# Performance work log

Hardware: AMD Instinct MI355X
Metric: run time of the kernel (lower is better)

The kernel has to match this reference:

```python
import jax, jax.numpy as jnp
import numpy as np
from jax import lax

PART = 224   # PART_IMAGE_SIZE
PAD = 224    # PAD_SIZE
TOPN = 4
IOU_THRESH = 0.25
N_ANCHORS = 1614


def _conv(x, w, b, stride, pad):
    y = lax.conv_general_dilated(x, w, (stride, stride), [(pad, pad), (pad, pad)],
                                 dimension_numbers=('NCHW', 'OIHW', 'NCHW'))
    return y + b[None, :, None, None]


def _iou(box, boxes):
    # box [4], boxes [N,4] as (y0,x0,y1,x1)
    yy0 = jnp.maximum(box[0], boxes[:, 0]); xx0 = jnp.maximum(box[1], boxes[:, 1])
    yy1 = jnp.minimum(box[2], boxes[:, 2]); xx1 = jnp.minimum(box[3], boxes[:, 3])
    inter = jnp.clip(yy1 - yy0, 0.0) * jnp.clip(xx1 - xx0, 0.0)
    a = (box[2] - box[0]) * (box[3] - box[1])
    areas = (boxes[:, 2] - boxes[:, 0]) * (boxes[:, 3] - boxes[:, 1])
    return inter / (a + areas - inter)


def _nms(scores, boxes):
    # hard NMS keeping TOPN boxes; returns indices [TOPN]
    valid = jnp.ones(scores.shape, dtype=bool)
    idxs = []
    for _ in range(TOPN):
        i = jnp.argmax(jnp.where(valid, scores, -jnp.inf))
        idxs.append(i)
        valid = valid & (_iou(boxes[i], boxes) <= IOU_THRESH)
    return jnp.stack(idxs)


def _crop_resize(img, box):
    # img [3,Hp,Wp] padded image, box [4] float; bilinear, align_corners=True,
    # matching F.interpolate(x_pad[:, :, y0:y1, x0:x1], (PART, PART))
    Hp, Wp = img.shape[1], img.shape[2]
    def coords(c0, c1, L):
        t = jnp.arange(PART, dtype=img.dtype) / (PART - 1)
        c = c0 + (c1 - 1.0 - c0) * t          # absolute source coordinate
        cf = jnp.floor(c)
        lo = jnp.clip(cf.astype(jnp.int32), 0, L - 1)
        hi = jnp.clip(lo + 1, 0, L - 1)
        return lo, hi, c - cf
    yl, yh, wy = coords(box[0], box[2], Hp)
    xl, xh, wx = coords(box[1], box[3], Wp)
    g = lambda yi, xi: img[:, yi[:, None], xi[None, :]]   # [3,PART,PART]
    return ((1 - wy)[:, None] * ((1 - wx) * g(yl, xl) + wx * g(yl, xh))
            + wy[:, None] * ((1 - wx) * g(yh, xl) + wx * g(yh, xh)))


def setup_inputs() -> dict:
    key = jax.random.key(0)
    ks = jax.random.split(key, 20)
    x = jax.random.uniform(ks[0], (16, 3, 448, 448), dtype=jnp.float32)
    rpn_feature = jax.random.normal(ks[1], (16, 2048, 14, 14), dtype=jnp.float32)
    # valid boxes inside the padded 896x896 image
    y0 = jax.random.randint(ks[2], (N_ANCHORS,), 0, 560)
    x0 = jax.random.randint(ks[3], (N_ANCHORS,), 0, 560)
    h = jax.random.randint(ks[4], (N_ANCHORS,), 32, 336)
    w = jax.random.randint(ks[5], (N_ANCHORS,), 32, 336)
    anchors = jnp.stack([y0, x0, jnp.minimum(y0 + h, 896), jnp.minimum(x0 + w, 896)], axis=1).astype(jnp.int32)
    s = 0.02
    inp = {
        'x': x, 'rpn_feature': rpn_feature, 'anchors': anchors,
        'w_down1': jax.random.normal(ks[6], (128, 2048, 3, 3), jnp.float32) * s,
        'b_down1': jnp.zeros((128,), jnp.float32),
        'w_down2': jax.random.normal(ks[7], (128, 128, 3, 3), jnp.float32) * s,
        'b_down2': jnp.zeros((128,), jnp.float32),
        'w_down3': jax.random.normal(ks[8], (128, 128, 3, 3), jnp.float32) * s,
        'b_down3': jnp.zeros((128,), jnp.float32),
        'w_tidy1': jax.random.normal(ks[9], (6, 128, 1, 1), jnp.float32) * s,
        'b_tidy1': jnp.zeros((6,), jnp.float32),
        'w_tidy2': jax.random.normal(ks[10], (6, 128, 1, 1), jnp.float32) * s,
        'b_tidy2': jnp.zeros((6,), jnp.float32),
        'w_tidy3': jax.random.normal(ks[11], (9, 128, 1, 1), jnp.float32) * s,
        'b_tidy3': jnp.zeros((9,), jnp.float32),
    }
    return inp


def reference(x, rpn_feature, anchors,
              w_down1, b_down1, w_down2, b_down2, w_down3, b_down3,
              w_tidy1, b_tidy1, w_tidy2, b_tidy2, w_tidy3, b_tidy3):
    B = x.shape[0]
    # ProposalNet
    d1 = jax.nn.relu(_conv(rpn_feature, w_down1, b_down1, 1, 1))   # [B,128,14,14]
    d2 = jax.nn.relu(_conv(d1, w_down2, b_down2, 2, 1))            # [B,128,7,7]
    d3 = jax.nn.relu(_conv(d2, w_down3, b_down3, 2, 1))            # [B,128,4,4]
    t1 = _conv(d1, w_tidy1, b_tidy1, 1, 0).reshape(B, -1)
    t2 = _conv(d2, w_tidy2, b_tidy2, 1, 0).reshape(B, -1)
    t3 = _conv(d3, w_tidy3, b_tidy3, 1, 0).reshape(B, -1)
    rpn_score = jnp.concatenate([t1, t2, t3], axis=1)              # [B, 1614]
    boxes = anchors.astype(x.dtype)                                # [N,4]
    top_n_index = jax.vmap(lambda s: _nms(s, boxes))(rpn_score)    # [B,TOPN]
    top_n_prob = jnp.take_along_axis(rpn_score, top_n_index, axis=1)
    x_pad = jnp.pad(x, ((0, 0), (0, 0), (PAD, PAD), (PAD, PAD)))   # [B,3,896,896]
    sel_boxes = boxes[top_n_index]                                 # [B,TOPN,4]
    part_imgs = jax.vmap(lambda img, bxs: jax.vmap(lambda b: _crop_resize(img, b))(bxs))(x_pad, sel_boxes)
    # part_imgs: [B,TOPN,3,PART,PART]
    return rpn_score, top_n_index, top_n_prob, part_imgs
```

## Files before the change

### kernel.cpp

```cpp
#include <hip/hip_runtime.h>
#include <hip/hip_bf16.h>

#define NB 16
#define NA 1614
#define NBP (NB * 196 * 128)

typedef __bf16 bf16x8 __attribute__((ext_vector_type(8)));
typedef float f32x4 __attribute__((ext_vector_type(4)));

__device__ __forceinline__ unsigned short f2bf(float v) {
  unsigned u = __float_as_uint(v);
  unsigned r = (u + 0x7FFFu + ((u >> 16) & 1u)) >> 16;
  return (unsigned short)r;
}
__device__ __forceinline__ float bf2f(unsigned short s) {
  return __uint_as_float(((unsigned)s) << 16);
}

__global__ __launch_bounds__(256)
void prep(const float* __restrict__ w, const float* __restrict__ in,
          unsigned short* __restrict__ wTh, unsigned short* __restrict__ wTl,
          unsigned short* __restrict__ aTh, unsigned short* __restrict__ aTl) {
  __shared__ float sbuf[32 * 289];
  const int bid = blockIdx.x;
  if (bid < 1024) {
    const int chunk = bid & 63, b = bid >> 6;
    const float* src = in + ((size_t)b * 2048 + chunk * 32) * 196;
#pragma unroll
    for (int r = 0; r < 7; r++) {
      int e = threadIdx.x + 256 * r;
      if (e < 1568) {
        int ic = e / 49, f = e - ic * 49;
        float4 v = ((const float4*)(src + (size_t)ic * 196))[f];
        float* d = sbuf + ic * 201 + f * 4;
        d[0] = v.x; d[1] = v.y; d[2] = v.z; d[3] = v.w;
      }
    }
    __syncthreads();
    unsigned short* oh = aTh + (size_t)bid * (196 * 32);
    unsigned short* ol = aTl + (size_t)bid * (196 * 32);
#pragma unroll
    for (int r = 0; r < 4; r++) {
      int e = threadIdx.x + 256 * r;
      if (e < 784) {
        int pos = e >> 2, part = e & 3;
        unsigned short hv[8], lv[8];
#pragma unroll
        for (int j = 0; j < 8; j++) {
          float v = sbuf[(part * 8 + j) * 201 + pos];
          unsigned short h = f2bf(v);
          hv[j] = h;
          lv[j] = f2bf(v - bf2f(h));
        }
        ((uint4*)oh)[e] = *(uint4*)hv;
        ((uint4*)ol)[e] = *(uint4*)lv;
      }
    }
  } else {
    const int bid2 = bid - 1024;
    const int ocg = bid2 & 3, ks = (bid2 >> 2) & 3, kcp = bid2 >> 4;
    const int oc0 = ocg * 32;
    const int ic0 = kcp * 128 + ks * 32;
#pragma unroll
    for (int r = 0; r < 9; r++) {
      int f = threadIdx.x + 256 * r;
      int o = f / 72, rem4 = f - o * 72;
      float4 v = *(const float4*)(w + ((size_t)(oc0 + o) * 2048 + ic0) * 9 + rem4 * 4);
      float* d = sbuf + o * 289 + rem4 * 4;
      d[0] = v.x; d[1] = v.y; d[2] = v.z; d[3] = v.w;
    }
    __syncthreads();
#pragma unroll
    for (int r = 0; r < 36; r++) {
      int e = threadIdx.x + 256 * r;
      int tap = e >> 10, rem = e & 1023;
      int o = rem >> 5, ic = rem & 31;
      float v = sbuf[o * 289 + ic * 9 + tap];
      unsigned short h = f2bf(v);
      size_t g2 = ((size_t)(kcp * 36 + tap * 4 + ks) << 12) + oc0 * 32 + rem;
      wTh[g2] = h;
      wTl[g2] = f2bf(v - bf2f(h));
    }
  }
}

#define LOADB(H, L, T, K)                                                     \
  {                                                                           \
    const size_t o_ = ((size_t)(kc * 36 + (T) * 4 + (K)) << 12) + bln;        \
    const unsigned short* ph_ = wTh + o_;                                     \
    const unsigned short* pq_ = wTl + o_;                                     \
    H[0] = *(const bf16x8*)(ph_);                                             \
    H[1] = *(const bf16x8*)(ph_ + 512);                                       \
    H[2] = *(const bf16x8*)(ph_ + 1024);                                      \
    H[3] = *(const bf16x8*)(ph_ + 1536);                                      \
    L[0] = *(const bf16x8*)(pq_);                                             \
    L[1] = *(const bf16x8*)(pq_ + 512);                                       \
    L[2] = *(const bf16x8*)(pq_ + 1024);                                      \
    L[3] = *(const bf16x8*)(pq_ + 1536);                                      \
  }

#define STEP(IT, BUH, BUL, BNH, BNL)                                          \
  {                                                                           \
    const int it_ = (IT);                                                     \
    const int ks_ = it_ / 9, tap_ = it_ - ks_ * 9;                            \
    const int dy_ = tap_ / 3 - 1;                                             \
    const int dx_ = tap_ - (tap_ / 3) * 3 - 1;                                \
    const int td_ = (ks_ * 196 + dy_ * 14 + dx_) * 4;        \
    bf16x8 afh[7], afl[7];                                                    \
    _Pragma("unroll") for (int mf = 0; mf < 7; mf++) {                        \
      uint4 vh_ = gA0h[td_ + aoff[mf]];                                       \
      uint4 vl_ = gA0l[td_ + aoff[mf]];                                       \
      bool ok_ = ((unsigned)(ay[mf] + dy_) < 14u) &&                          \
                 ((unsigned)(ax[mf] + dx_) < 14u);                            \
      if (!ok_) {                                                             \
        vh_.x = 0u; vh_.y = 0u; vh_.z = 0u; vh_.w = 0u;                       \
        vl_.x = 0u; vl_.y = 0u; vl_.z = 0u; vl_.w = 0u;                       \
      }                                                                       \
      afh[mf] = *(const bf16x8*)&vh_;                                         \
      afl[mf] = *(const bf16x8*)&vl_;                                         \
    }                                                                         \
    {             \
      const int ni_ = (it_ < 35) ? it_ + 1 : 35;                              \
      const int nk_ = ni_ / 9, nt_ = ni_ - nk_ * 9;                           \
      LOADB(BNH, BNL, nt_, nk_);                                              \
    }                                                                         \
    _Pragma("unroll") for (int mf = 0; mf < 7; mf++)                          \
      _Pragma("unroll") for (int nf = 0; nf < 4; nf++)                        \
        acc[mf][nf] = __builtin_amdgcn_mfma_f32_16x16x32_bf16(afh[mf], BUH[nf], acc[mf][nf], 0, 0, 0); \
    _Pragma("unroll") for (int mf = 0; mf < 7; mf++)                          \
      _Pragma("unroll") for (int nf = 0; nf < 4; nf++)                        \
        acc[mf][nf] = __builtin_amdgcn_mfma_f32_16x16x32_bf16(afl[mf], BUH[nf], acc[mf][nf], 0, 0, 0); \
    _Pragma("unroll") for (int mf = 0; mf < 7; mf++)                          \
      _Pragma("unroll") for (int nf = 0; nf < 4; nf++)                        \
        acc[mf][nf] = __builtin_amdgcn_mfma_f32_16x16x32_bf16(afh[mf], BUL[nf], acc[mf][nf], 0, 0, 0); \
  }

__global__ __launch_bounds__(256, 1)
void conv1_mfma(const unsigned short* __restrict__ aTh, const unsigned short* __restrict__ aTl,
                const unsigned short* __restrict__ wTh, const unsigned short* __restrict__ wTl,
                float* __restrict__ p1) {
  const int bid = blockIdx.x;
  const int kc = bid & 15;
  const int b  = bid >> 4;
  const int tid = threadIdx.x;
  const int wid = tid >> 6, lane = tid & 63;
  const int wm = wid & 1, wn = wid >> 1;
  const int q = lane >> 4, ln = lane & 15;

  int ay[7], ax[7], aoff[7];
#pragma unroll
  for (int mf = 0; mf < 7; mf++) {
    int row = wm * 112 + mf * 16 + ln;
    int v = (row < 196);
    int y = v ? row / 14 : 0;
    int x = v ? (row - y * 14) : 0;
    if (!v) y = 0;
    ay[mf] = y; ax[mf] = x;
    aoff[mf] = (y * 14 + x) * 4 + q;
  }
  const int bln = (wn * 64 + ln) * 32 + q * 8;

  const uint4* gA0h = (const uint4*)(aTh + (size_t)(b * 64 + kc * 4) * 6272);
  const uint4* gA0l = (const uint4*)(aTl + (size_t)(b * 64 + kc * 4) * 6272);

  f32x4 acc[7][4];
#pragma unroll
  for (int mf = 0; mf < 7; mf++)
#pragma unroll
    for (int nf = 0; nf < 4; nf++) acc[mf][nf] = (f32x4){0.f, 0.f, 0.f, 0.f};

  bf16x8 b0h[4], b0l[4], b1h[4], b1l[4];
  LOADB(b0h, b0l, 0, 0);

  for (int it = 0; it < 36; it += 2) {
    STEP(it,     b0h, b0l, b1h, b1l);
    STEP(it + 1, b1h, b1l, b0h, b0l);
  }

  float* pk = p1 + ((size_t)kc * NB + b) * 196 * 128;
#pragma unroll
  for (int mf = 0; mf < 7; mf++) {
    const int row0 = wm * 112 + mf * 16 + q * 4;
#pragma unroll
    for (int nf = 0; nf < 4; nf++) {
      const int oc = wn * 64 + nf * 16 + ln;
#pragma unroll
      for (int r = 0; r < 4; r++) {
        const int row = row0 + r;
        if (row < 196) pk[(size_t)row * 128 + oc] = acc[mf][nf][r];
      }
    }
  }
}

__global__ __launch_bounds__(256)
void conv1_finish_p(const float* __restrict__ p1, const float* __restrict__ bias,
                    float* __restrict__ d1) {
  __shared__ float s[28 * 132];
  const int bid = blockIdx.x;
  const int pt = bid % 7, b = bid / 7;
  const int tid = threadIdx.x;
#pragma unroll
  for (int r = 0; r < 4; r++) {
    int u = tid + 256 * r;
    if (u < 896) {
      int pos = u >> 5, oc4 = u & 31;
      const float* base = p1 + ((size_t)(b * 196 + pt * 28 + pos)) * 128 + oc4 * 4;
      float4 sum = ((const float4*)bias)[oc4];
#pragma unroll
      for (int k = 0; k < 16; k++) {
        float4 v = *(const float4*)(base + (size_t)k * NBP);
        sum.x += v.x; sum.y += v.y; sum.z += v.z; sum.w += v.w;
      }
      sum.x = fmaxf(sum.x, 0.f); sum.y = fmaxf(sum.y, 0.f);
      sum.z = fmaxf(sum.z, 0.f); sum.w = fmaxf(sum.w, 0.f);
      *(float4*)(s + pos * 132 + oc4 * 4) = sum;
    }
  }
  __syncthreads();
#pragma unroll
  for (int r = 0; r < 4; r++) {
    int u = tid + 256 * r;
    if (u < 896) {
      int oc = u / 7, f = u - oc * 7;
      float4 v;
      v.x = s[(f * 4 + 0) * 132 + oc];
      v.y = s[(f * 4 + 1) * 132 + oc];
      v.z = s[(f * 4 + 2) * 132 + oc];
      v.w = s[(f * 4 + 3) * 132 + oc];
      *(float4*)(d1 + ((size_t)b * 128 + oc) * 196 + pt * 28 + f * 4) = v;
    }
  }
}

__global__ void conv2_part(const float* __restrict__ d1, const float* __restrict__ w,
                           float* __restrict__ p2) {
  const int bid = blockIdx.x;
  const int kc = bid & 3, oct = (bid >> 2) & 3, b = bid >> 4;
  const int ic0 = kc * 32, oc0 = oct * 32;
  const int tid = threadIdx.x;
  const int ocl = tid >> 3, rw = tid & 7;

  __shared__ float s_in[32 * 320];
  __shared__ float s_w[32 * 324];

#pragma unroll
  for (int r = 0; r < 32; r++) {
    const int e = tid + 256 * r;
    const int ch = e >> 8, idx = e & 255;
    const int tr = idx >> 4, tc = idx & 15;
    const int iy = tr - 1, ix = tc - 1;
    float v = 0.f;
    if ((unsigned)iy < 14u && (unsigned)ix < 14u)
      v = d1[((size_t)b * 128 + ic0 + ch) * 196 + iy * 14 + ix];
    s_in[ch * 320 + tr * 20 + tc] = v;
  }
#pragma unroll
  for (int r = 0; r < 36; r++) {
    const int e = tid + 256 * r;
    const int oc = e / 288, rem = e - oc * 288;
    const int ch = rem / 9, tap = rem - ch * 9;
    s_w[ch * 324 + tap * 36 + oc] =
        w[(size_t)(oc0 + oc) * 1152 + (size_t)ic0 * 9 + rem];
  }
  __syncthreads();

  if (rw < 7) {
    float acc[7] = {};
    for (int ic = 0; ic < 32; ic++) {
      const float* wrow = s_w + ic * 324 + ocl;
      const float* irow = s_in + ic * 320;
#pragma unroll
      for (int ky = 0; ky < 3; ky++) {
        const float* r = irow + (2 * rw + ky) * 20;
        const float4 f0 = *(const float4*)(r);
        const float4 f1 = *(const float4*)(r + 4);
        const float4 f2 = *(const float4*)(r + 8);
        const float4 f3 = *(const float4*)(r + 12);
        const float ev[8] = {f0.x, f0.z, f1.x, f1.z, f2.x, f2.z, f3.x, f3.z};
        const float od[7] = {f0.y, f0.w, f1.y, f1.w, f2.y, f2.w, f3.y};
        const float w0 = wrow[(ky * 3 + 0) * 36];
        const float w1 = wrow[(ky * 3 + 1) * 36];
        const float w2 = wrow[(ky * 3 + 2) * 36];
#pragma unroll
        for (int x = 0; x < 7; x++)
          acc[x] = fmaf(w0, ev[x], fmaf(w1, od[x], fmaf(w2, ev[x + 1], acc[x])));
      }
    }
    float* po = p2 + (((size_t)kc * NB + b) * 128 + oc0 + ocl) * 49 + rw * 7;
#pragma unroll
    for (int x = 0; x < 7; x++) po[x] = acc[x];
  }
}

__global__ void conv2_finish(const float* __restrict__ p2, const float* __restrict__ bias,
                             float* __restrict__ d2) {
  const int i = blockIdx.x * 256 + threadIdx.x;
  if (i >= NB * 128 * 49) return;
  const int oc = (i / 49) & 127;
  float s = bias[oc];
#pragma unroll
  for (int k = 0; k < 4; k++) s += p2[(size_t)k * (NB * 128 * 49) + i];
  d2[i] = fmaxf(s, 0.f);
}

__global__ void conv3_part(const float* __restrict__ d2, const float* __restrict__ w,
                           float* __restrict__ p3) {
  const int bid = blockIdx.x;
  const int kc = bid & 1, oct = (bid >> 1) & 7, b = bid >> 4;
  const int ic0 = kc * 64, oc0 = oct * 16;
  const int tid = threadIdx.x;
  const int oc = tid >> 4, p = tid & 15;
  const int y = p >> 2, x = p & 3;

  __shared__ float s_in[64 * 108];
  __shared__ float s_w[64 * 144];

#pragma unroll
  for (int r = 0; r < 21; r++) {
    const int e = tid + 256 * r;
    if (e < 64 * 81) {
      const int ch = e / 81, idx = e - ch * 81;
      const int tr = idx / 9, tc = idx - tr * 9;
      const int iy = tr - 1, ix = tc - 1;
      float v = 0.f;
      if ((unsigned)iy < 7u && (unsigned)ix < 7u)
        v = d2[((size_t)b * 128 + ic0 + ch) * 49 + iy * 7 + ix];
      s_in[ch * 108 + tr * 12 + tc] = v;
    }
  }
#pragma unroll
  for (int r = 0; r < 36; r++) {
    const int e = tid + 256 * r;
    const int o = e / 576, rem = e - o * 576;
    const int ch = rem / 9, tap = rem - ch * 9;
    s_w[ch * 144 + tap * 16 + o] =
        w[(size_t)(oc0 + o) * 1152 + (size_t)ic0 * 9 + rem];
  }
  __syncthreads();

  float acc = 0.f;
  for (int ic = 0; ic < 64; ic++) {
    const float* wrow = s_w + ic * 144 + oc;
    const float* irow = s_in + ic * 108 + 2 * y * 12 + 2 * x;
#pragma unroll
    for (int ky = 0; ky < 3; ky++)
#pragma unroll
      for (int kx = 0; kx < 3; kx++)
        acc = fmaf(wrow[(ky * 3 + kx) * 16], irow[ky * 12 + kx], acc);
  }
  p3[(((size_t)kc * NB + b) * 128 + oc0 + oc) * 16 + p] = acc;
}

__global__ __launch_bounds__(256, 1)
void score_nms(const float* __restrict__ d1, const float* __restrict__ d2,
               const float* __restrict__ p3, const float* __restrict__ bd3,
               const float* __restrict__ w1, const float* __restrict__ b1,
               const float* __restrict__ w2, const float* __restrict__ b2,
               const float* __restrict__ w3, const float* __restrict__ b3,
               const int* __restrict__ anchors, float* __restrict__ score,
               float* __restrict__ out_idx, float* __restrict__ out_prob,
               float* __restrict__ sel) {
  __shared__ float s_in[32 * 200];
  __shared__ float s_w[21 * 128];
  __shared__ float s_b[21];
  __shared__ float s_sc[NA];
  __shared__ float s_bx[NA * 4];
  __shared__ float r_s[256];
  __shared__ int r_i[256];
  const int b = blockIdx.x, tid = threadIdx.x;

  for (int i = tid; i < 768; i += 256) s_w[i] = w1[i];
  for (int i = tid; i < 768; i += 256) s_w[768 + i] = w2[i];
  for (int i = tid; i < 1152; i += 256) s_w[1536 + i] = w3[i];
  if (tid < 21) s_b[tid] = (tid < 6) ? b1[tid] : (tid < 12) ? b2[tid - 6] : b3[tid - 12];
  for (int i = tid; i < NA; i += 256) {
    s_bx[i * 4 + 0] = (float)anchors[i * 4 + 0];
    s_bx[i * 4 + 1] = (float)anchors[i * 4 + 1];
    s_bx[i * 4 + 2] = (float)anchors[i * 4 + 2];
    s_bx[i * 4 + 3] = (float)anchors[i * 4 + 3];
  }

  float acc[5] = {0.f, 0.f, 0.f, 0.f, 0.f};
  for (int chunk = 0; chunk < 4; chunk++) {
    __syncthreads();
    const float* src = d1 + ((size_t)b * 128 + chunk * 32) * 196;
#pragma unroll
    for (int r = 0; r < 7; r++) {
      int e = tid + 256 * r;
      if (e < 1568) {
        int ic = e / 49, f = e - ic * 49;
        *(float4*)(s_in + ic * 200 + f * 4) = ((const float4*)(src + (size_t)ic * 196))[f];
      }
    }
    __syncthreads();
#pragma unroll
    for (int k = 0; k < 5; k++) {
      int j = tid + 256 * k;
      if (j < 1176) {
        int oc = j / 196, p = j - oc * 196;
        const float* wr = s_w + oc * 128 + chunk * 32;
        float s = acc[k];
#pragma unroll
        for (int ic = 0; ic < 32; ic++) s = fmaf(wr[ic], s_in[ic * 200 + p], s);
        acc[k] = s;
      }
    }
  }
#pragma unroll
  for (int k = 0; k < 5; k++) {
    int j = tid + 256 * k;
    if (j < 1176) {
      int oc = j / 196;
      float s = acc[k] + s_b[oc];
      s_sc[j] = s;
      score[b * NA + j] = s;
    }
  }

  __syncthreads();
  {
    const float* src = d2 + (size_t)b * 6272;
#pragma unroll
    for (int r = 0; r < 7; r++) {
      int e = tid + 256 * r;
      if (e < 1568) *(float4*)(s_in + e * 4) = ((const float4*)src)[e];
    }
  }
  __syncthreads();
#pragma unroll
  for (int k = 0; k < 2; k++) {
    int jj = tid + 256 * k;
    if (jj < 294) {
      int oc = jj / 49, p = jj - oc * 49;
      const float* wr = s_w + 768 + oc * 128;
      float s = s_b[6 + oc];
#pragma unroll 8
      for (int ic = 0; ic < 128; ic++) s = fmaf(wr[ic], s_in[ic * 49 + p], s);
      s_sc[1176 + jj] = s;
      score[b * NA + 1176 + jj] = s;
    }
  }

  __syncthreads();
  {
    const float4* s0 = (const float4*)(p3 + (size_t)b * 2048);
    const float4* s1 = (const float4*)(p3 + 32768 + (size_t)b * 2048);
#pragma unroll
    for (int r = 0; r < 2; r++) {
      int e = tid + 256 * r;
      if (e < 512) {
        float4 a = s0[e], c = s1[e];
        float bb = bd3[e >> 2];
        float4 v;
        v.x = fmaxf(a.x + c.x + bb, 0.f);
        v.y = fmaxf(a.y + c.y + bb, 0.f);
        v.z = fmaxf(a.z + c.z + bb, 0.f);
        v.w = fmaxf(a.w + c.w + bb, 0.f);
        *(float4*)(s_in + e * 4) = v;
      }
    }
  }
  __syncthreads();
  if (tid < 144) {
    int oc = tid >> 4, p = tid & 15;
    const float* wr = s_w + 1536 + oc * 128;
    float s = s_b[12 + oc];
#pragma unroll 8
    for (int ic = 0; ic < 128; ic++) s = fmaf(wr[ic], s_in[ic * 16 + p], s);
    s_sc[1470 + tid] = s;
    score[b * NA + 1470 + tid] = s;
  }
  __syncthreads();

  for (int t = 0; t < 4; t++) {
    float bs = -__builtin_inff();
    int bi = NA;
    for (int i = tid; i < NA; i += 256) {
      float s = s_sc[i];
      if (s > bs || (s == bs && i < bi)) { bs = s; bi = i; }
    }
    r_s[tid] = bs; r_i[tid] = bi;
    __syncthreads();
    for (int off = 128; off > 0; off >>= 1) {
      if (tid < off) {
        float s2 = r_s[tid + off]; int i2 = r_i[tid + off];
        if (s2 > r_s[tid] || (s2 == r_s[tid] && i2 < r_i[tid])) { r_s[tid] = s2; r_i[tid] = i2; }
      }
      __syncthreads();
    }
    const int idx = r_i[0];
    const float by0 = s_bx[idx * 4 + 0], bx0 = s_bx[idx * 4 + 1];
    const float by1 = s_bx[idx * 4 + 2], bx1 = s_bx[idx * 4 + 3];
    if (tid == 0) {
      out_idx[b * 4 + t] = (float)idx;
      out_prob[b * 4 + t] = s_sc[idx];
      sel[(b * 4 + t) * 4 + 0] = by0;
      sel[(b * 4 + t) * 4 + 1] = bx0;
      sel[(b * 4 + t) * 4 + 2] = by1;
      sel[(b * 4 + t) * 4 + 3] = bx1;
    }
    __syncthreads();
    const float a = (by1 - by0) * (bx1 - bx0);
    for (int i = tid; i < NA; i += 256) {
      float cy0 = s_bx[i * 4 + 0], cx0 = s_bx[i * 4 + 1];
      float cy1 = s_bx[i * 4 + 2], cx1 = s_bx[i * 4 + 3];
      float yy0 = fmaxf(by0, cy0), xx0 = fmaxf(bx0, cx0);
      float yy1 = fminf(by1, cy1), xx1 = fminf(bx1, cx1);
      float inter = fmaxf(yy1 - yy0, 0.f) * fmaxf(xx1 - xx0, 0.f);
      float ar = (cy1 - cy0) * (cx1 - cx0);
      float iou = inter / (a + ar - inter);
      if (iou > 0.25f) s_sc[i] = -__builtin_inff();
    }
    __syncthreads();
  }
}

__global__ void crop_kernel(const float* __restrict__ x, const float* __restrict__ sel,
                            float* __restrict__ out) {
  int i4 = blockIdx.x * 256 + threadIdx.x;
  const int total4 = NB * 4 * 3 * 224 * 56;
  if (i4 >= total4) return;
  int px0 = (i4 % 56) * 4;
  int t = i4 / 56;
  int py = t % 224; t /= 224;
  int ch = t % 3;  t /= 3;
  int n  = t % 4;
  int b  = t / 4;

  const float* bx = sel + (b * 4 + n) * 4;
  const float y0 = bx[0], x0 = bx[1], y1 = bx[2], x1 = bx[3];

  float ty = (float)py / 223.0f;
  float cy = y0 + (y1 - 1.0f - y0) * ty;
  float cyf = floorf(cy);
  int ylo = (int)cyf; ylo = ylo < 0 ? 0 : (ylo > 895 ? 895 : ylo);
  int yhi = ylo + 1 > 895 ? 895 : ylo + 1;
  float wy = cy - cyf;

  const float* img = x + ((size_t)b * 3 + ch) * 448 * 448;
  auto g = [&](int yy, int xx) -> float {
    yy -= 224; xx -= 224;
    if ((unsigned)yy < 448u && (unsigned)xx < 448u)
      return img[(size_t)yy * 448 + xx];
    return 0.f;
  };

  float4 res;
  float* rp = &res.x;
#pragma unroll
  for (int k = 0; k < 4; k++) {
    float tx = (float)(px0 + k) / 223.0f;
    float cx = x0 + (x1 - 1.0f - x0) * tx;
    float cxf = floorf(cx);
    int xlo = (int)cxf; xlo = xlo < 0 ? 0 : (xlo > 895 ? 895 : xlo);
    int xhi = xlo + 1 > 895 ? 895 : xlo + 1;
    float wx = cx - cxf;
    float v00 = g(ylo, xlo), v01 = g(ylo, xhi);
    float v10 = g(yhi, xlo), v11 = g(yhi, xhi);
    rp[k] = (1.f - wy) * ((1.f - wx) * v00 + wx * v01) +
            wy * ((1.f - wx) * v10 + wx * v11);
  }
  *(float4*)(out + (size_t)i4 * 4) = res;
}

extern "C" void kernel_launch(void* const* d_in, const int* in_sizes, int n_in,
                              void* d_out, int out_size, void* d_ws, size_t ws_size,
                              hipStream_t stream) {
  const float* x    = (const float*)d_in[0];
  const float* rpn  = (const float*)d_in[1];
  const int*   anc  = (const int*)d_in[2];
  const float* w_d1 = (const float*)d_in[3];
  const float* b_d1 = (const float*)d_in[4];
  const float* w_d2 = (const float*)d_in[5];
  const float* b_d2 = (const float*)d_in[6];
  const float* w_d3 = (const float*)d_in[7];
  const float* b_d3 = (const float*)d_in[8];
  const float* w_t1 = (const float*)d_in[9];
  const float* b_t1 = (const float*)d_in[10];
  const float* w_t2 = (const float*)d_in[11];
  const float* b_t2 = (const float*)d_in[12];
  const float* w_t3 = (const float*)d_in[13];
  const float* b_t3 = (const float*)d_in[14];

  float* out = (float*)d_out;
  float* ws = (float*)d_ws;

  float* d1  = ws;
  float* d2  = d1 + 401408;
  float* d3  = d2 + 100352;
  float* sel = d3 + 32768;
  float* p2  = sel + 256;
  float* p3  = p2 + 401408;
  unsigned short* wTh = (unsigned short*)(p3 + 65536);
  unsigned short* wTl = wTh + 2359296;
  unsigned short* aTh = wTl + 2359296;
  unsigned short* aTl = aTh + 6422528;

  float* score    = out;
  float* out_idx  = out + 25824;
  float* out_prob = out + 25888;
  float* parts    = out + 25952;
  float* p1       = parts;

  prep<<<dim3(1280), dim3(256), 0, stream>>>(w_d1, rpn, wTh, wTl, aTh, aTl);
  conv1_mfma<<<dim3(256), dim3(256), 0, stream>>>(aTh, aTl, wTh, wTl, p1);
  conv1_finish_p<<<dim3(112), dim3(256), 0, stream>>>(p1, b_d1, d1);
  conv2_part<<<dim3(256), dim3(256), 0, stream>>>(d1, w_d2, p2);
  conv2_finish<<<dim3(392), dim3(256), 0, stream>>>(p2, b_d2, d2);
  conv3_part<<<dim3(256), dim3(256), 0, stream>>>(d2, w_d3, p3);
  score_nms<<<dim3(16), dim3(256), 0, stream>>>(d1, d2, p3, b_d3, w_t1, b_t1, w_t2, b_t2,
                                                w_t3, b_t3, anc, score, out_idx, out_prob, sel);
  crop_kernel<<<dim3(9408), dim3(256), 0, stream>>>(x, sel, parts);
}
```

Baseline: 313.3 us.

## Stage conv1 activations in padded LDS and switch to 32x32 MFMA with 512 threads

```diff
diff --git a/kernel.cpp b/kernel.cpp
--- a/kernel.cpp
+++ b/kernel.cpp
@@ -6,7 +6,7 @@
 #define NBP (NB * 196 * 128)
 
 typedef __bf16 bf16x8 __attribute__((ext_vector_type(8)));
-typedef float f32x4 __attribute__((ext_vector_type(4)));
+typedef float f32x16 __attribute__((ext_vector_type(16)));
 
 __device__ __forceinline__ unsigned short f2bf(float v) {
   unsigned u = __float_as_uint(v);
@@ -74,29 +74,33 @@
     for (int r = 0; r < 36; r++) {
       int e = threadIdx.x + 256 * r;
       int tap = e >> 10, rem = e & 1023;
-      int o = rem >> 5, ic = rem & 31;
+      int k16 = (rem >> 9) & 1, khalf = (rem >> 8) & 1;
+      int o = (rem >> 3) & 31, j = rem & 7;
+      int ic = k16 * 16 + khalf * 8 + j;
       float v = sbuf[o * 289 + ic * 9 + tap];
       unsigned short h = f2bf(v);
-      size_t g2 = ((size_t)(kcp * 36 + tap * 4 + ks) << 12) + oc0 * 32 + rem;
+      size_t g2 = ((size_t)(kcp * 36 + tap * 4 + ks) << 12)
+                  + k16 * 2048 + khalf * 1024 + (size_t)(oc0 + o) * 8 + j;
       wTh[g2] = h;
       wTl[g2] = f2bf(v - bf2f(h));
     }
   }
 }
 
+#define APL 2192
+#define ABUF (4 * APL)
+
 #define LOADB(H, L, T, K)                                                     \
   {                                                                           \
-    const size_t o_ = ((size_t)(kc * 36 + (T) * 4 + (K)) << 12) + bln;        \
-    const unsigned short* ph_ = wTh + o_;                                     \
-    const unsigned short* pq_ = wTl + o_;                                     \
-    H[0] = *(const bf16x8*)(ph_);                                             \
-    H[1] = *(const bf16x8*)(ph_ + 512);                                       \
-    H[2] = *(const bf16x8*)(ph_ + 1024);                                      \
-    H[3] = *(const bf16x8*)(ph_ + 1536);                                      \
-    L[0] = *(const bf16x8*)(pq_);                                             \
-    L[1] = *(const bf16x8*)(pq_ + 512);                                       \
-    L[2] = *(const bf16x8*)(pq_ + 1024);                                      \
-    L[3] = *(const bf16x8*)(pq_ + 1536);                                      \
+    const size_t o_ = ((size_t)(kc * 36 + (T) * 4 + (K)) << 12) + blane;      \
+    H[0] = *(const bf16x8*)(wTh + o_);                        \
+    H[1] = *(const bf16x8*)(wTh + o_ + 256);                  \
+    H[2] = *(const bf16x8*)(wTh + o_ + 2048);                 \
+    H[3] = *(const bf16x8*)(wTh + o_ + 2304);                 \
+    L[0] = *(const bf16x8*)(wTl + o_);                                        \
+    L[1] = *(const bf16x8*)(wTl + o_ + 256);                                  \
+    L[2] = *(const bf16x8*)(wTl + o_ + 2048);                                 \
+    L[3] = *(const bf16x8*)(wTl + o_ + 2304);                                 \
   }
 
 #define STEP(IT, BUH, BUL, BNH, BNL)                                          \
@@ -105,37 +109,63 @@
     const int ks_ = it_ / 9, tap_ = it_ - ks_ * 9;                            \
     const int dy_ = tap_ / 3 - 1;                                             \
     const int dx_ = tap_ - (tap_ / 3) * 3 - 1;                                \
-    const int td_ = (ks_ * 196 + dy_ * 14 + dx_) * 4;        \
-    bf16x8 afh[7], afl[7];                                                    \
-    _Pragma("unroll") for (int mf = 0; mf < 7; mf++) {                        \
-      uint4 vh_ = gA0h[td_ + aoff[mf]];                                       \
-      uint4 vl_ = gA0l[td_ + aoff[mf]];                                       \
-      bool ok_ = ((unsigned)(ay[mf] + dy_) < 14u) &&                          \
-                 ((unsigned)(ax[mf] + dx_) < 14u);                            \
-      if (!ok_) {                                                             \
-        vh_.x = 0u; vh_.y = 0u; vh_.z = 0u; vh_.w = 0u;                       \
-        vl_.x = 0u; vl_.y = 0u; vl_.z = 0u; vl_.w = 0u;                       \
-      }                                                                       \
-      afh[mf] = *(const bf16x8*)&vh_;                                         \
-      afl[mf] = *(const bf16x8*)&vl_;                                         \
+    const int t8_ = dy_ * 136 + dx_ * 8;                                      \
+    const unsigned short* pah_ = sAh + (ks_ & 1) * ABUF + khoff;              \
+    const unsigned short* pal_ = sAl + (ks_ & 1) * ABUF + khoff;              \
+    bf16x8 afh[2][2], afl[2][2];                                              \
+    _Pragma("unroll") for (int f = 0; f < 2; f++) {                           \
+      const int ab_ = abase[f] + t8_;                                         \
+      afh[f][0] = *(const bf16x8*)(pah_ + ab_);                               \
+      afh[f][1] = *(const bf16x8*)(pah_ + 2 * APL + ab_);                     \
+      afl[f][0] = *(const bf16x8*)(pal_ + ab_);                               \
+      afl[f][1] = *(const bf16x8*)(pal_ + 2 * APL + ab_);                     \
     }                                                                         \
     {             \
       const int ni_ = (it_ < 35) ? it_ + 1 : 35;                              \
       const int nk_ = ni_ / 9, nt_ = ni_ - nk_ * 9;                           \
       LOADB(BNH, BNL, nt_, nk_);                                              \
     }                                                                         \
-    _Pragma("unroll") for (int mf = 0; mf < 7; mf++)                          \
-      _Pragma("unroll") for (int nf = 0; nf < 4; nf++)                        \
-        acc[mf][nf] = __builtin_amdgcn_mfma_f32_16x16x32_bf16(afh[mf], BUH[nf], acc[mf][nf], 0, 0, 0); \
-    _Pragma("unroll") for (int mf = 0; mf < 7; mf++)                          \
-      _Pragma("unroll") for (int nf = 0; nf < 4; nf++)                        \
-        acc[mf][nf] = __builtin_amdgcn_mfma_f32_16x16x32_bf16(afl[mf], BUH[nf], acc[mf][nf], 0, 0, 0); \
-    _Pragma("unroll") for (int mf = 0; mf < 7; mf++)                          \
-      _Pragma("unroll") for (int nf = 0; nf < 4; nf++)                        \
-        acc[mf][nf] = __builtin_amdgcn_mfma_f32_16x16x32_bf16(afh[mf], BUL[nf], acc[mf][nf], 0, 0, 0); \
-  }
-
-__global__ __launch_bounds__(256, 1)
+    if (ks_ < 3) {  \
+      if (tap_ == 2) {                                                        \
+        const uint4* gh_ = (const uint4*)(aTh + (size_t)(b * 64 + kc * 4 + ks_ + 1) * 6272); \
+        const uint4* gl_ = (const uint4*)(aTl + (size_t)(b * 64 + kc * 4 + ks_ + 1) * 6272); \
+        sgh0 = gh_[tid]; sgl0 = gl_[tid];                                     \
+        if (tid + 512 < 784) { sgh1 = gh_[tid + 512]; sgl1 = gl_[tid + 512]; } \
+      }                                                                       \
+      if (tap_ == 3) {                                                        \
+        const int pos_ = tid >> 2, part_ = tid & 3;                           \
+        const int py_ = pos_ / 14, px_ = pos_ - py_ * 14;                     \
+        const int d_ = (((ks_ + 1) & 1) ? ABUF : 0) + part_ * APL             \
+                       + (py_ + 1) * 136 + (px_ + 1) * 8;                     \
+        *(uint4*)(sAh + d_) = sgh0;                                           \
+        *(uint4*)(sAl + d_) = sgl0;                                           \
+      }                                                                       \
+      if (tap_ == 4 && tid + 512 < 784) {                                     \
+        const int e_ = tid + 512;                                             \
+        const int pos_ = e_ >> 2, part_ = e_ & 3;                             \
+        const int py_ = pos_ / 14, px_ = pos_ - py_ * 14;                     \
+        const int d_ = (((ks_ + 1) & 1) ? ABUF : 0) + part_ * APL             \
+                       + (py_ + 1) * 136 + (px_ + 1) * 8;                     \
+        *(uint4*)(sAh + d_) = sgh1;                                           \
+        *(uint4*)(sAl + d_) = sgl1;                                           \
+      }                                                                       \
+    }                                                                         \
+    _Pragma("unroll") for (int k = 0; k < 2; k++)                             \
+      _Pragma("unroll") for (int f = 0; f < 2; f++)                           \
+        _Pragma("unroll") for (int nf = 0; nf < 2; nf++)                      \
+          acc[f][nf] = __builtin_amdgcn_mfma_f32_32x32x16_bf16(afh[f][k], BUH[k * 2 + nf], acc[f][nf], 0, 0, 0); \
+    _Pragma("unroll") for (int k = 0; k < 2; k++)                             \
+      _Pragma("unroll") for (int f = 0; f < 2; f++)                           \
+        _Pragma("unroll") for (int nf = 0; nf < 2; nf++)                      \
+          acc[f][nf] = __builtin_amdgcn_mfma_f32_32x32x16_bf16(afl[f][k], BUH[k * 2 + nf], acc[f][nf], 0, 0, 0); \
+    _Pragma("unroll") for (int k = 0; k < 2; k++)                             \
+      _Pragma("unroll") for (int f = 0; f < 2; f++)                           \
+        _Pragma("unroll") for (int nf = 0; nf < 2; nf++)                      \
+          acc[f][nf] = __builtin_amdgcn_mfma_f32_32x32x16_bf16(afh[f][k], BUL[k * 2 + nf], acc[f][nf], 0, 0, 0); \
+    if (tap_ == 8) __syncthreads();                                           \
+  }
+
+__global__ __launch_bounds__(512)
 void conv1_mfma(const unsigned short* __restrict__ aTh, const unsigned short* __restrict__ aTl,
                 const unsigned short* __restrict__ wTh, const unsigned short* __restrict__ wTl,
                 float* __restrict__ p1) {
@@ -144,33 +174,61 @@
   const int b  = bid >> 4;
   const int tid = threadIdx.x;
   const int wid = tid >> 6, lane = tid & 63;
-  const int wm = wid & 1, wn = wid >> 1;
-  const int q = lane >> 4, ln = lane & 15;
-
-  int ay[7], ax[7], aoff[7];
-#pragma unroll
-  for (int mf = 0; mf < 7; mf++) {
-    int row = wm * 112 + mf * 16 + ln;
-    int v = (row < 196);
-    int y = v ? row / 14 : 0;
-    int x = v ? (row - y * 14) : 0;
-    if (!v) y = 0;
-    ay[mf] = y; ax[mf] = x;
-    aoff[mf] = (y * 14 + x) * 4 + q;
-  }
-  const int bln = (wn * 64 + ln) * 32 + q * 8;
-
-  const uint4* gA0h = (const uint4*)(aTh + (size_t)(b * 64 + kc * 4) * 6272);
-  const uint4* gA0l = (const uint4*)(aTl + (size_t)(b * 64 + kc * 4) * 6272);
-
-  f32x4 acc[7][4];
-#pragma unroll
-  for (int mf = 0; mf < 7; mf++)
-#pragma unroll
-    for (int nf = 0; nf < 4; nf++) acc[mf][nf] = (f32x4){0.f, 0.f, 0.f, 0.f};
-
+  const int wm = wid & 3, wn = wid >> 2;
+  const int l31 = lane & 31, lh = lane >> 5;
+
+  __shared__ unsigned short sAh[2 * ABUF];
+  __shared__ unsigned short sAl[2 * ABUF];
+
+  for (int e = tid; e < 8768; e += 512) {
+    ((unsigned int*)sAh)[e] = 0u;
+    ((unsigned int*)sAl)[e] = 0u;
+  }
+
+  const int khoff = lh * APL;
+  int abase[2];
+#pragma unroll
+  for (int f = 0; f < 2; f++) {
+    int row = wm * 64 + f * 32 + l31;
+    if (row < 196) {
+      int y = row / 14, x = row - y * 14;
+      abase[f] = (y + 1) * 136 + (x + 1) * 8;
+    } else {
+      abase[f] = 136 + 8;
+    }
+  }
+  const int blane = lh * 1024 + wn * 512 + l31 * 8;
+
+  f32x16 acc[2][2];
+#pragma unroll
+  for (int f = 0; f < 2; f++)
+#pragma unroll
+    for (int nf = 0; nf < 2; nf++)
+#pragma unroll
+      for (int r = 0; r < 16; r++) acc[f][nf][r] = 0.f;
+
+  uint4 sgh0 = {}, sgl0 = {}, sgh1 = {}, sgl1 = {};
+
+  __syncthreads();
+
+  {
+    const uint4* gh = (const uint4*)(aTh + (size_t)(b * 64 + kc * 4) * 6272);
+    const uint4* gl = (const uint4*)(aTl + (size_t)(b * 64 + kc * 4) * 6272);
+#pragma unroll
+    for (int r = 0; r < 2; r++) {
+      int e = tid + 512 * r;
+      if (e < 784) {
+        int pos = e >> 2, part = e & 3;
+        int py = pos / 14, px = pos - py * 14;
+        int d = part * APL + (py + 1) * 136 + (px + 1) * 8;
+        *(uint4*)(sAh + d) = gh[e];
+        *(uint4*)(sAl + d) = gl[e];
+      }
+    }
+  }
   bf16x8 b0h[4], b0l[4], b1h[4], b1l[4];
   LOADB(b0h, b0l, 0, 0);
+  __syncthreads();
 
   for (int it = 0; it < 36; it += 2) {
     STEP(it,     b0h, b0l, b1h, b1l);
@@ -179,15 +237,14 @@
 
   float* pk = p1 + ((size_t)kc * NB + b) * 196 * 128;
 #pragma unroll
-  for (int mf = 0; mf < 7; mf++) {
-    const int row0 = wm * 112 + mf * 16 + q * 4;
-#pragma unroll
-    for (int nf = 0; nf < 4; nf++) {
-      const int oc = wn * 64 + nf * 16 + ln;
-#pragma unroll
-      for (int r = 0; r < 4; r++) {
-        const int row = row0 + r;
-        if (row < 196) pk[(size_t)row * 128 + oc] = acc[mf][nf][r];
+  for (int f = 0; f < 2; f++) {
+#pragma unroll
+    for (int nf = 0; nf < 2; nf++) {
+      const int oc = wn * 64 + nf * 32 + l31;
+#pragma unroll
+      for (int r = 0; r < 16; r++) {
+        const int row = wm * 64 + f * 32 + (r & 3) + 8 * (r >> 2) + 4 * lh;
+        if (row < 196) pk[(size_t)row * 128 + oc] = acc[f][nf][r];
       }
     }
   }
@@ -604,7 +661,7 @@
   float* p1       = parts;
 
   prep<<<dim3(1280), dim3(256), 0, stream>>>(w_d1, rpn, wTh, wTl, aTh, aTl);
-  conv1_mfma<<<dim3(256), dim3(256), 0, stream>>>(aTh, aTl, wTh, wTl, p1);
+  conv1_mfma<<<dim3(256), dim3(512), 0, stream>>>(aTh, aTl, wTh, wTl, p1);
   conv1_finish_p<<<dim3(112), dim3(256), 0, stream>>>(p1, b_d1, d1);
   conv2_part<<<dim3(256), dim3(256), 0, stream>>>(d1, w_d2, p2);
   conv2_finish<<<dim3(392), dim3(256), 0, stream>>>(p2, b_d2, d2);
```

Measured after the change: 282.9 us. 1.11x faster.
